# Kernel tuning notes

Hardware: AMD Instinct MI355X
Metric: run time of the kernel (lower is better)

The kernel has to match this reference:

```python
import jax, jax.numpy as jnp
import numpy as np
import math

H = 1024      # d_input / d_output channels
N = 64        # d_state (diagonal SSM size)
L = 2048      # kernel / sequence length
DT_MIN, DT_MAX = 0.001, 0.1
HIGH_STAB, LOW_STAB = -0.9, -0.8


def setup_inputs() -> dict:
    key = jax.random.key(0)
    k1, k2, k3, k4 = jax.random.split(key, 4)
    # log_dt ~ U[log(dt_min), log(dt_max)]
    log_dt = jax.random.uniform(k1, (H,), dtype=jnp.float32) \
        * (math.log(DT_MAX) - math.log(DT_MIN)) + math.log(DT_MIN)
    # C ~ complex normal, stored as real pairs (H, N, 2) like torch.view_as_real
    C = jax.random.normal(k2, (H, N, 2), dtype=jnp.float32)
    # Diagonal A: Re(A) uniform in [high_stability, low_stability] (stable),
    # Im(A) random; stored as real pairs (N, 2). A is a frozen buffer.
    a_re = jax.random.uniform(k3, (N,), dtype=jnp.float32) * (LOW_STAB - HIGH_STAB) + HIGH_STAB
    a_im = jax.random.normal(k4, (N,), dtype=jnp.float32) * math.pi
    A = jnp.stack([a_re, a_im], axis=-1)
    return {"log_dt": log_dt, "C": C, "A": A, "input_length": L}


def reference(log_dt, C, A, input_length):
    # log_dt: (H,) float32; C: (H,N,2) float32; A: (N,2) float32
    dt = jnp.exp(log_dt)                                   # (H,)
    Cc = (C[..., 0] + 1j * C[..., 1]).astype(jnp.complex64)  # (H, N)
    Ac = (A[..., 0] + 1j * A[..., 1]).astype(jnp.complex64)  # (N,)
    dtA = dt[:, None].astype(jnp.complex64) * Ac[None, :]  # (H, N)
    # Vandermonde-style kernel: exp(dtA * l) for l in [0, L)
    l = jnp.arange(input_length, dtype=jnp.float32).astype(jnp.complex64)  # (L,)
    Kexp = jnp.exp(dtA[:, :, None] * l[None, None, :])     # (H, N, L) complex64
    Cmod = Cc * (jnp.exp(dtA) - 1.0) / Ac                  # (H, N)
    K = 2.0 * jnp.einsum('hn,hnl->hl', Cmod, Kexp).real    # (H, L) float32
    return K
```

## Files before the change

### kernel.cpp

```cpp
#include <hip/hip_runtime.h>

#define H 1024
#define N 64
#define L 2048
#define TPB 256
#define KK (L / TPB)

#define INV2PI 0.15915494309189535f

typedef float f32x2 __attribute__((ext_vector_type(2)));


__device__ __forceinline__ f32x2 pk_add(f32x2 a, f32x2 b) {
    f32x2 d;
    asm("v_pk_add_f32 %0, %1, %2" : "=v"(d) : "v"(a), "v"(b));
    return d;
}

__device__ __forceinline__ f32x2 cmul(f32x2 w, f32x2 s) {
    f32x2 t, r;
    asm("v_pk_mul_f32 %0, %1, %2 op_sel_hi:[1,0]"
        : "=v"(t) : "v"(w), "v"(s));
    asm("v_pk_fma_f32 %0, %1, %2, %3 op_sel:[1,1,0] op_sel_hi:[0,1,1] neg_lo:[1,0,0]"
        : "=v"(r) : "v"(w), "v"(s), "v"(t));
    return r;
}

__global__ __launch_bounds__(TPB) void s4d_fused(const float* __restrict__ log_dt,
                                                 const float* __restrict__ Cv,
                                                 const float* __restrict__ Av,
                                                 float* __restrict__ out)
{
    __shared__ float4 p1[N];
    __shared__ f32x2 p2[N];

    const int h = blockIdx.x;
    const int t = threadIdx.x;

    if (t < N) {
        float dt = __expf(log_dt[h]);
        float2 a2 = ((const float2*)Av)[t];
        float ar = a2.x, ai = a2.y;
        float dr = dt * ar;
        float direv = dt * ai * INV2PI;

        float mr  = __expf(dr);
        float rev = direv - floorf(direv);
        float rr = mr * __builtin_amdgcn_cosf(rev);
        float ri = mr * __builtin_amdgcn_sinf(rev);

        float ms   = __expf(dr * (float)TPB);
        float revs = direv * (float)TPB;
        revs -= floorf(revs);
        float sr = ms * __builtin_amdgcn_cosf(revs);
        float si = ms * __builtin_amdgcn_sinf(revs);

        float2 c2 = ((const float2*)Cv)[h * N + t];
        float er = rr - 1.0f, ei = ri;
        float tr = c2.x * er - c2.y * ei;
        float ti = c2.x * ei + c2.y * er;
        float inv = 2.0f / (ar * ar + ai * ai);
        f32x2 cm;
        cm.x = (tr * ar + ti * ai) * inv;
        cm.y = (ti * ar - tr * ai) * inv;

        p1[t] = make_float4(dr, direv, sr, si);
        p2[t] = cm;
    }
    __syncthreads();

    f32x2 acc[KK];
#pragma unroll
    for (int k = 0; k < KK; ++k) acc[k] = (f32x2)(0.0f);

    const float tf = (float)t;

#pragma unroll 2
    for (int n = 0; n < N; ++n) {
        float4 a   = p1[n];
        f32x2 cmv  = p2[n];

        float m   = __expf(a.x * tf);
        float rev = a.y * tf;
        rev -= floorf(rev);
        f32x2 e;
        e.x = m * __builtin_amdgcn_cosf(rev);
        e.y = m * __builtin_amdgcn_sinf(rev);
        f32x2 w = cmul(e, cmv);

        f32x2 s;
        s.x = a.z; s.y = a.w;

#pragma unroll
        for (int k = 0; k < KK; ++k) {
            acc[k] = pk_add(acc[k], w);
            w = cmul(w, s);
        }
    }

    float* o = out + h * L + t;
#pragma unroll
    for (int k = 0; k < KK; ++k) o[k * TPB] = acc[k].x;
}

extern "C" void kernel_launch(void* const* d_in, const int* in_sizes, int n_in,
                              void* d_out, int out_size, void* d_ws, size_t ws_size,
                              hipStream_t stream) {
    const float* log_dt = (const float*)d_in[0];
    const float* Cv     = (const float*)d_in[1];
    const float* Av     = (const float*)d_in[2];
    float* out          = (float*)d_out;

    s4d_fused<<<H, TPB, 0, stream>>>(log_dt, Cv, Av, out);
}
```

Before: 79.69 us.

## Replace per-thread transcendental with split 16x16 power tables in shared memory

Each thread previously evaluated one exp/cos/sin per state element. Now the block precomputes two 16-entry tables per state, low powers e^{dtA*j} and C-scaled high powers e^{dtA*16j}, so each thread forms its starting term with a single complex multiply of two LDS entries. This removes transcendental work from the 64-iteration main loop, but adds a larger setup phase that every thread takes part in and more LDS reads per iteration. The unroll factor of the n loop is also raised from 2 to 4.

```diff
diff --git a/kernel.cpp b/kernel.cpp
--- a/kernel.cpp
+++ b/kernel.cpp
@@ -26,46 +26,60 @@
     return r;
 }
 
+__device__ __forceinline__ f32x2 cexp_rev(float mag_arg, float rev_arg) {
+    float m = __expf(mag_arg);
+    float rv = rev_arg - floorf(rev_arg);
+    f32x2 e;
+    e.x = m * __builtin_amdgcn_cosf(rv);
+    e.y = m * __builtin_amdgcn_sinf(rv);
+    return e;
+}
+
 __global__ __launch_bounds__(TPB) void s4d_fused(const float* __restrict__ log_dt,
                                                  const float* __restrict__ Cv,
                                                  const float* __restrict__ Av,
                                                  float* __restrict__ out)
 {
-    __shared__ float4 p1[N];
-    __shared__ f32x2 p2[N];
+    __shared__ f32x2 W16[N][16];
+    __shared__ f32x2 E1t[N][16];
+    __shared__ f32x2 Sv[N];
 
     const int h = blockIdx.x;
     const int t = threadIdx.x;
 
-    if (t < N) {
+    {
+        const int n  = t >> 2;
+        const int j0 = (t & 3) << 2;
         float dt = __expf(log_dt[h]);
-        float2 a2 = ((const float2*)Av)[t];
-        float ar = a2.x, ai = a2.y;
-        float dr = dt * ar;
-        float direv = dt * ai * INV2PI;
 
-        float mr  = __expf(dr);
-        float rev = direv - floorf(direv);
-        float rr = mr * __builtin_amdgcn_cosf(rev);
-        float ri = mr * __builtin_amdgcn_sinf(rev);
+        float2 a2 = ((const float2*)Av)[n];
+        float dr    = dt * a2.x;
+        float direv = dt * a2.y * INV2PI;
 
-        float ms   = __expf(dr * (float)TPB);
-        float revs = direv * (float)TPB;
-        revs -= floorf(revs);
-        float sr = ms * __builtin_amdgcn_cosf(revs);
-        float si = ms * __builtin_amdgcn_sinf(revs);
-
-        float2 c2 = ((const float2*)Cv)[h * N + t];
-        float er = rr - 1.0f, ei = ri;
+        f32x2 r1 = cexp_rev(dr, direv);
+        float2 c2 = ((const float2*)Cv)[h * N + n];
+        float er = r1.x - 1.0f, ei = r1.y;
         float tr = c2.x * er - c2.y * ei;
         float ti = c2.x * ei + c2.y * er;
-        float inv = 2.0f / (ar * ar + ai * ai);
+        float inv = 2.0f / (a2.x * a2.x + a2.y * a2.y);
         f32x2 cm;
-        cm.x = (tr * ar + ti * ai) * inv;
-        cm.y = (ti * ar - tr * ai) * inv;
+        cm.x = (tr * a2.x + ti * a2.y) * inv;
+        cm.y = (ti * a2.x - tr * a2.y) * inv;
 
-        p1[t] = make_float4(dr, direv, sr, si);
-        p2[t] = cm;
+#pragma unroll
+        for (int jj = 0; jj < 4; ++jj) {
+            float fj = (float)(j0 + jj);
+            E1t[n][j0 + jj] = cexp_rev(dr * fj, direv * fj);
+            float fg = fj * 16.0f;
+            W16[n][j0 + jj] = cmul(cexp_rev(dr * fg, direv * fg), cm);
+        }
+
+        if (t < N) {
+            float2 a2b = ((const float2*)Av)[t];
+            float drb = dt * a2b.x;
+            float dib = dt * a2b.y * INV2PI;
+            Sv[t] = cexp_rev(drb * 256.0f, dib * 256.0f);
+        }
     }
     __syncthreads();
 
@@ -73,23 +87,15 @@
 #pragma unroll
     for (int k = 0; k < KK; ++k) acc[k] = (f32x2)(0.0f);
 
-    const float tf = (float)t;
+    const int jhi = t >> 4;
+    const int jlo = t & 15;
 
-#pragma unroll 2
+#pragma unroll 4
     for (int n = 0; n < N; ++n) {
-        float4 a   = p1[n];
-        f32x2 cmv  = p2[n];
-
-        float m   = __expf(a.x * tf);
-        float rev = a.y * tf;
-        rev -= floorf(rev);
-        f32x2 e;
-        e.x = m * __builtin_amdgcn_cosf(rev);
-        e.y = m * __builtin_amdgcn_sinf(rev);
-        f32x2 w = cmul(e, cmv);
-
-        f32x2 s;
-        s.x = a.z; s.y = a.w;
+        f32x2 w16 = W16[n][jhi];
+        f32x2 e1  = E1t[n][jlo];
+        f32x2 s   = Sv[n];
+        f32x2 w = cmul(e1, w16);
 
 #pragma unroll
         for (int k = 0; k < KK; ++k) {
```

Result: faster. 75.49 us (-5.3%).
